# Kernel optimization log

Measured on AMD Instinct MI355X. Metric: run time of the kernel, lower is better.

## Reference

```python
import jax, jax.numpy as jnp
import numpy as np

N_NODES = 262144
N_EDGES = 4194304
F_IN = 4
HID = 8
HEADS = 2
N_CLS = 3
NEG_SLOPE = 0.2
EPS = 1e-16


def setup_inputs() -> dict:
    key = jax.random.key(0)
    k = jax.random.split(key, 8)
    x = jax.random.normal(k[0], (N_NODES, F_IN), dtype=jnp.float32)
    edge_index = jax.random.randint(k[1], (2, N_EDGES), 0, N_NODES, dtype=jnp.int64)
    # layer 1: in=4, heads=2, out=8, concat -> 16
    W1 = jax.random.normal(k[2], (F_IN, HEADS * HID), dtype=jnp.float32) * 0.5
    a_src1 = jax.random.normal(k[3], (HEADS, HID), dtype=jnp.float32) * 0.5
    a_dst1 = jax.random.normal(k[4], (HEADS, HID), dtype=jnp.float32) * 0.5
    # layer 2: in=16, heads=1, out=3, mean (concat=False)
    W2 = jax.random.normal(k[5], (HEADS * HID, 1 * N_CLS), dtype=jnp.float32) * 0.5
    a_src2 = jax.random.normal(k[6], (1, N_CLS), dtype=jnp.float32) * 0.5
    a_dst2 = jax.random.normal(k[7], (1, N_CLS), dtype=jnp.float32) * 0.5
    return {"x": x, "edge_index": edge_index, "W1": W1, "a_src1": a_src1,
            "a_dst1": a_dst1, "W2": W2, "a_src2": a_src2, "a_dst2": a_dst2}


def _gat_conv(x, src, dst, W, a_src, a_dst, heads, out_dim, concat):
    N = x.shape[0]
    h = (x @ W).reshape(N, heads, out_dim)            # [N,H,F]
    al_s = jnp.sum(h * a_src[None], axis=-1)          # [N,H]
    al_d = jnp.sum(h * a_dst[None], axis=-1)          # [N,H]
    e = jax.nn.leaky_relu(al_s[src] + al_d[dst], NEG_SLOPE)  # [E,H]
    m = jax.ops.segment_max(e, dst, num_segments=N)   # [N,H]
    ex = jnp.exp(e - m[dst])
    denom = jax.ops.segment_sum(ex, dst, num_segments=N)
    alpha = ex / (denom[dst] + EPS)                   # [E,H]
    out = jax.ops.segment_sum(h[src] * alpha[:, :, None], dst, num_segments=N)  # [N,H,F]
    if concat:
        return out.reshape(N, heads * out_dim)
    return out.mean(axis=1)


def reference(x, edge_index, W1, a_src1, a_dst1, W2, a_src2, a_dst2):
    N = x.shape[0]
    loops = jnp.arange(N, dtype=edge_index.dtype)
    src = jnp.concatenate([edge_index[0], loops])
    dst = jnp.concatenate([edge_index[1], loops])
    h = _gat_conv(x, src, dst, W1, a_src1, a_dst1, HEADS, HID, True)
    h = jax.nn.relu(h)
    out = _gat_conv(h, src, dst, W2, a_src2, a_dst2, 1, N_CLS, False)
    return jax.nn.softmax(out, axis=-1)
```

## Files before the change

### kernel.cpp

```cpp
#include <hip/hip_runtime.h>
#include <cstdint>
#include <cstddef>


#define NN 262144
#define NE 4194304
#define NB 1024
#define NPB 256
#define EB 8192
#define NBLK (NE / EB)
#define CAPB 4608
#define BT 512
#define ILEN (CAPB / BT)

__device__ __forceinline__ float lrelu(float v) { return v > 0.0f ? v : 0.2f * v; }
__device__ __forceinline__ float rfl(float v) {
    return __int_as_float(__builtin_amdgcn_readfirstlane(__float_as_int(v)));
}

__global__ __launch_bounds__(512, 8) void k_bin(const void* __restrict__ ei,
                                                unsigned* __restrict__ binned,
                                                unsigned* __restrict__ runs)
{
    __shared__ unsigned stage[EB];
    __shared__ int h[NB];
    __shared__ int wtot[8];
    __shared__ int sfmt;
    int t = threadIdx.x, blk = blockIdx.x;
    for (int i = t; i < NB; i += 512) h[i] = 0;
    if (t == 0) {
        const unsigned* u = (const unsigned*)ei;
        int is64 = 1;
        for (int k = 0; k < 64; ++k)
            if (u[2 * k + 1] != 0u) { is64 = 0; break; }
        sfmt = is64;
    }
    __syncthreads();
    int f64 = sfmt;
    size_t base = (size_t)blk * EB;
    int dd[16], ss[16];
    if (f64) {
        const long long* ps = (const long long*)ei;
        const long long* pd = ps + NE;
#pragma unroll
        for (int r = 0; r < 16; ++r) {
            size_t e = base + (size_t)r * 512 + t;
            ss[r] = (int)ps[e];
            dd[r] = (int)pd[e];
            atomicAdd(&h[dd[r] >> 8], 1);
        }
    } else {
        const int* ps = (const int*)ei;
        const int* pd = ps + NE;
#pragma unroll
        for (int r = 0; r < 16; ++r) {
            size_t e = base + (size_t)r * 512 + t;
            ss[r] = ps[e];
            dd[r] = pd[e];
            atomicAdd(&h[dd[r] >> 8], 1);
        }
    }
    __syncthreads();
    int c0 = h[2 * t], c1 = h[2 * t + 1];
    int own = c0 + c1;
    int lane = t & 63, w = t >> 6;
    int p = own;
#pragma unroll
    for (int o = 1; o < 64; o <<= 1) {
        int v = __shfl_up(p, o);
        if (lane >= o) p += v;
    }
    if (lane == 63) wtot[w] = p;
    __syncthreads();
    int bw = 0;
#pragma unroll
    for (int q = 0; q < 8; ++q) bw += (q < w) ? wtot[q] : 0;
    int e0 = bw + p - own;
    h[2 * t] = e0;
    h[2 * t + 1] = e0 + c0;
    ((uint2*)(runs + (size_t)blk * NB))[t] =
        make_uint2((unsigned)e0 | ((unsigned)c0 << 16),
                   (unsigned)(e0 + c0) | ((unsigned)c1 << 16));
    __syncthreads();
#pragma unroll
    for (int r = 0; r < 16; ++r) {
        int pos = atomicAdd(&h[dd[r] >> 8], 1);
        stage[pos] = ((unsigned)(dd[r] & 255) << 18) | (unsigned)ss[r];
    }
    __syncthreads();
    uint4* dst4 = (uint4*)(binned + (size_t)blk * EB);
    const uint4* src4 = (const uint4*)stage;
    for (int i = t; i < EB / 4; i += 512) dst4[i] = src4[i];
}

__global__ __launch_bounds__(256) void k_truns(const unsigned* __restrict__ runs,
                                               unsigned* __restrict__ runsT)
{
    __shared__ unsigned tile[32][33];
    int tx = threadIdx.x & 31, ty = threadIdx.x >> 5;
    int bx = blockIdx.x * 32;
    int by = blockIdx.y * 32;
#pragma unroll
    for (int j = 0; j < 4; ++j)
        tile[ty + 8 * j][tx] = runs[(size_t)(by + ty + 8 * j) * NB + bx + tx];
    __syncthreads();
#pragma unroll
    for (int j = 0; j < 4; ++j)
        runsT[(size_t)(bx + ty + 8 * j) * NBLK + by + tx] = tile[tx][ty + 8 * j];
}

__global__ __launch_bounds__(BT, 8) void k_l1f(
    const float4* __restrict__ x4,
    const float* __restrict__ W1, const float* __restrict__ as1, const float* __restrict__ ad1,
    const unsigned* __restrict__ binned, const unsigned* __restrict__ runsT,
    const float* __restrict__ W2, const float* __restrict__ as2, const float* __restrict__ ad2,
    int* __restrict__ ssrc, int2* __restrict__ rse,
    float4* __restrict__ p4, float* __restrict__ ald2)
{
    __shared__ unsigned stage[CAPB];
    __shared__ int pf[NBLK + 1];
    __shared__ int gb[NBLK];
    __shared__ int hist[NPB], off[NPB], rsL[NPB], reL[NPB];
    __shared__ int wt1[8], wt2[4];
    __shared__ float sW1[64], sW2[48], sf[16], sa2[6];
    int t = threadIdx.x, b = blockIdx.x;
    if (t < 64) sW1[t] = W1[t];
    if (t >= 64 && t < 112) sW2[t - 64] = W2[t - 64];
    if (t >= 128 && t < 144) {
        int i = t - 128;
        int kind = i >> 3, head = (i >> 2) & 1, f = i & 3;
        const float* a = kind ? ad1 : as1;
        float v = 0.f;
        for (int j = 0; j < 8; ++j)
            v += W1[f * 16 + head * 8 + j] * a[head * 8 + j];
        sf[i] = v;
    }
    if (t >= 144 && t < 147) sa2[t - 144] = as2[t - 144];
    if (t >= 147 && t < 150) sa2[t - 144] = ad2[t - 147];
    if (t < NPB) hist[t] = 0;
    unsigned rn = runsT[(size_t)b * NBLK + t];
    int cnt = (int)(rn >> 16);
    int lane = t & 63, w = t >> 6;
    int p = cnt;
#pragma unroll
    for (int o = 1; o < 64; o <<= 1) {
        int v = __shfl_up(p, o);
        if (lane >= o) p += v;
    }
    if (lane == 63) wt1[w] = p;
    __syncthreads();
    int bw = 0;
#pragma unroll
    for (int q = 0; q < 8; ++q) bw += (q < w) ? wt1[q] : 0;
    int incl = bw + p;
    int excl = incl - cnt;
    pf[t] = excl;
    if (t == BT - 1) pf[NBLK] = incl;
    gb[t] = t * EB + (int)(rn & 0xFFFF);
    __syncthreads();
    int n = pf[NBLK] < CAPB ? pf[NBLK] : CAPB;
    unsigned pk[ILEN];
#pragma unroll
    for (int k = 0; k < ILEN; ++k) {
        int i = k * BT + t;
        pk[k] = 0xFFFFFFFFu;
        if (i < n) {
            int r = 0;
#pragma unroll
            for (int s = 256; s > 0; s >>= 1)
                if (pf[r + s] <= i) r += s;
            unsigned pp = binned[gb[r] + (i - pf[r])];
            pk[k] = pp;
            atomicAdd(&hist[pp >> 18], 1);
        }
    }
    __syncthreads();
    int ownN = (t < NPB) ? hist[t] : 0;
    int pN = ownN;
#pragma unroll
    for (int o = 1; o < 64; o <<= 1) {
        int v = __shfl_up(pN, o);
        if (lane >= o) pN += v;
    }
    if (t < NPB && lane == 63) wt2[w] = pN;
    __syncthreads();
    int s0 = b * CAPB;
    if (t < NPB) {
        int baseN = 0;
#pragma unroll
        for (int q = 0; q < 4; ++q) baseN += (q < w) ? wt2[q] : 0;
        int exclN = baseN + pN - ownN;
        off[t] = exclN;
        rsL[t] = exclN;
        reL[t] = exclN + ownN;
        rse[b * NPB + t] = make_int2(s0 + exclN, s0 + exclN + ownN);
    }
    __syncthreads();
#pragma unroll
    for (int k = 0; k < ILEN; ++k) {
        unsigned pp = pk[k];
        if (pp != 0xFFFFFFFFu) {
            int pos = atomicAdd(&off[pp >> 18], 1);
            stage[pos] = pp & 0x3FFFFu;
        }
    }
    __syncthreads();
    for (int i = t; i < n; i += BT) ssrc[s0 + i] = (int)stage[i];
    float ws00 = rfl(sf[0]),  ws01 = rfl(sf[1]),  ws02 = rfl(sf[2]),  ws03 = rfl(sf[3]);
    float ws10 = rfl(sf[4]),  ws11 = rfl(sf[5]),  ws12 = rfl(sf[6]),  ws13 = rfl(sf[7]);
    float wd00 = rfl(sf[8]),  wd01 = rfl(sf[9]),  wd02 = rfl(sf[10]), wd03 = rfl(sf[11]);
    float wd10 = rfl(sf[12]), wd11 = rfl(sf[13]), wd12 = rfl(sf[14]), wd13 = rfl(sf[15]);
    int nl = t >> 1, sub = t & 1;
    int node = b * NPB + nl;
    float4 xn = x4[node];
    float ald0  = xn.x * wd00 + xn.y * wd01 + xn.z * wd02 + xn.w * wd03;
    float ald1v = xn.x * wd10 + xn.y * wd11 + xn.z * wd12 + xn.w * wd13;
    float den0 = 0.f, den1 = 0.f;
    float wa00 = 0.f, wa01 = 0.f, wa02 = 0.f, wa03 = 0.f;
    float wa10 = 0.f, wa11 = 0.f, wa12 = 0.f, wa13 = 0.f;
    if (sub == 0) {
        float as0s = xn.x * ws00 + xn.y * ws01 + xn.z * ws02 + xn.w * ws03;
        float as1s = xn.x * ws10 + xn.y * ws11 + xn.z * ws12 + xn.w * ws13;
        float x0 = __expf(lrelu(as0s + ald0));
        float x1 = __expf(lrelu(as1s + ald1v));
        den0 = x0; den1 = x1;
        wa00 = x0 * xn.x; wa01 = x0 * xn.y; wa02 = x0 * xn.z; wa03 = x0 * xn.w;
        wa10 = x1 * xn.x; wa11 = x1 * xn.y; wa12 = x1 * xn.z; wa13 = x1 * xn.w;
    }
    int j = rsL[nl] + sub, je = reL[nl];
    float4 xsA, xsB;
    if (j < je) xsA = x4[stage[j]];
    if (j + 2 < je) xsB = x4[stage[j + 2]];
    while (j < je) {
        float4 xs = xsA;
        xsA = xsB;
        if (j + 4 < je) xsB = x4[stage[j + 4]];
        float as0 = xs.x * ws00 + xs.y * ws01 + xs.z * ws02 + xs.w * ws03;
        float as1v = xs.x * ws10 + xs.y * ws11 + xs.z * ws12 + xs.w * ws13;
        float e0 = __expf(lrelu(as0 + ald0));
        float e1 = __expf(lrelu(as1v + ald1v));
        den0 += e0; den1 += e1;
        wa00 += e0 * xs.x; wa01 += e0 * xs.y; wa02 += e0 * xs.z; wa03 += e0 * xs.w;
        wa10 += e1 * xs.x; wa11 += e1 * xs.y; wa12 += e1 * xs.z; wa13 += e1 * xs.w;
        j += 2;
    }
    den0 += __shfl_xor(den0, 1);  den1 += __shfl_xor(den1, 1);
    wa00 += __shfl_xor(wa00, 1);  wa01 += __shfl_xor(wa01, 1);
    wa02 += __shfl_xor(wa02, 1);  wa03 += __shfl_xor(wa03, 1);
    wa10 += __shfl_xor(wa10, 1);  wa11 += __shfl_xor(wa11, 1);
    wa12 += __shfl_xor(wa12, 1);  wa13 += __shfl_xor(wa13, 1);
    if (sub == 0) {
        float i0 = 1.0f / (den0 + 1e-16f);
        float i1 = 1.0f / (den1 + 1e-16f);
        float p0 = 0.f, p1 = 0.f, p2 = 0.f;
#pragma unroll
        for (int f = 0; f < 8; ++f) {
            float num0 = wa00 * sW1[f]      + wa01 * sW1[16 + f]
                       + wa02 * sW1[32 + f] + wa03 * sW1[48 + f];
            float num1 = wa10 * sW1[8 + f]  + wa11 * sW1[24 + f]
                       + wa12 * sW1[40 + f] + wa13 * sW1[56 + f];
            float o0 = fmaxf(num0 * i0, 0.f);
            float o1 = fmaxf(num1 * i1, 0.f);
            p0 += o0 * sW2[f * 3 + 0] + o1 * sW2[(8 + f) * 3 + 0];
            p1 += o0 * sW2[f * 3 + 1] + o1 * sW2[(8 + f) * 3 + 1];
            p2 += o0 * sW2[f * 3 + 2] + o1 * sW2[(8 + f) * 3 + 2];
        }
        float als2v = p0 * sa2[0] + p1 * sa2[1] + p2 * sa2[2];
        float ald2v = p0 * sa2[3] + p1 * sa2[4] + p2 * sa2[5];
        p4[node] = make_float4(als2v, p0, p1, p2);
        ald2[node] = ald2v;
    }
}

__global__ __launch_bounds__(BT, 8) void k_l2agg(
    const float4* __restrict__ p4, const float* __restrict__ ald2,
    const int2* __restrict__ rse, const int* __restrict__ ssrc,
    float* __restrict__ out)
{
    __shared__ unsigned stage[CAPB];
    __shared__ int rsL[NPB], reL[NPB];
    __shared__ int sn;
    int t = threadIdx.x, b = blockIdx.x;
    int s0 = b * CAPB;
    if (t < NPB) {
        int2 se = rse[b * NPB + t];
        rsL[t] = se.x - s0;
        reL[t] = se.y - s0;
        if (t == NPB - 1) sn = se.y - s0;
    }
    __syncthreads();
    int n = sn;
    for (int i = t; i < n; i += BT) stage[i] = (unsigned)ssrc[s0 + i];
    __syncthreads();
    int nl = t >> 1, sub = t & 1;
    int node = b * NPB + nl;
    float aldi = ald2[node];
    float den = 0.f, a0 = 0.f, a1 = 0.f, a2 = 0.f;
    if (sub == 0) {
        float4 pn = p4[node];
        float xv = __expf(lrelu(pn.x + aldi));
        den = xv; a0 = xv * pn.y; a1 = xv * pn.z; a2 = xv * pn.w;
    }
    int j = rsL[nl] + sub, je = reL[nl];
    float4 pA, pB;
    if (j < je) pA = p4[stage[j]];
    if (j + 2 < je) pB = p4[stage[j + 2]];
    while (j < je) {
        float4 pv = pA;
        pA = pB;
        if (j + 4 < je) pB = p4[stage[j + 4]];
        float e = __expf(lrelu(pv.x + aldi));
        den += e; a0 += e * pv.y; a1 += e * pv.z; a2 += e * pv.w;
        j += 2;
    }
    den += __shfl_xor(den, 1);
    a0 += __shfl_xor(a0, 1);
    a1 += __shfl_xor(a1, 1);
    a2 += __shfl_xor(a2, 1);
    if (sub == 0) {
        float inv = 1.0f / (den + 1e-16f);
        float l0 = a0 * inv, l1 = a1 * inv, l2 = a2 * inv;
        float m = fmaxf(l0, fmaxf(l1, l2));
        float e0 = __expf(l0 - m), e1 = __expf(l1 - m), e2 = __expf(l2 - m);
        float is = 1.0f / (e0 + e1 + e2);
        out[(size_t)node * 3 + 0] = e0 * is;
        out[(size_t)node * 3 + 1] = e1 * is;
        out[(size_t)node * 3 + 2] = e2 * is;
    }
}

extern "C" void kernel_launch(void* const* d_in, const int* in_sizes, int n_in,
                              void* d_out, int out_size, void* d_ws, size_t ws_size,
                              hipStream_t stream)
{
    const float* x   = (const float*)d_in[0];
    const void*  ei  = d_in[1];
    const float* W1  = (const float*)d_in[2];
    const float* as1 = (const float*)d_in[3];
    const float* ad1 = (const float*)d_in[4];
    const float* W2  = (const float*)d_in[5];
    const float* as2 = (const float*)d_in[6];
    const float* ad2 = (const float*)d_in[7];
    float* out = (float*)d_out;

    char* ws = (char*)d_ws;
    size_t off = 0;
    auto carve = [&](size_t bytes) {
        void* p = ws + off;
        off = (off + bytes + 255) & ~(size_t)255;
        return p;
    };
    unsigned* binned = (unsigned*)carve((size_t)NE * 4);
    unsigned* runs   = (unsigned*)carve((size_t)NBLK * NB * 4);
    unsigned* runsT  = (unsigned*)carve((size_t)NB * NBLK * 4);
    int*      ssrc   = (int*)carve((size_t)NB * CAPB * 4);
    int2*     rse    = (int2*)carve((size_t)NN * 8);
    float4*   p4     = (float4*)carve((size_t)NN * 16);
    float*    ald2   = (float*)carve((size_t)NN * 4);

    k_bin<<<NBLK, 512, 0, stream>>>(ei, binned, runs);
    k_truns<<<dim3(NB / 32, NBLK / 32), 256, 0, stream>>>(runs, runsT);
    k_l1f<<<NB, BT, 0, stream>>>((const float4*)x, W1, as1, ad1, binned, runsT,
                                 W2, as2, ad2, ssrc, rse, p4, ald2);
    k_l2agg<<<NB, BT, 0, stream>>>(p4, ald2, rse, ssrc, out);
}
```

Baseline: 86.78 us.

## Sort nodes by in-degree within each block to balance per-wave edge loops

Each block now buckets its 256 nodes by in-degree (capped at 63) with a shared-memory histogram and prefix scan. Threads process nodes in that sorted order in both the layer-1 fused kernel and the layer-2 aggregation kernel, so lanes within a wavefront have similar loop trip counts and less divergence. The local node id is packed into the top 8 bits of the range start, and layer 2 finds the segment end with an atomicMax. This adds extra syncs, atomics and an indirection, and it assumes segment offsets fit in 24 bits.

```diff
diff --git a/kernel.cpp b/kernel.cpp
--- a/kernel.cpp
+++ b/kernel.cpp
@@ -122,9 +122,11 @@
     __shared__ int gb[NBLK];
     __shared__ int hist[NPB], off[NPB], rsL[NPB], reL[NPB];
     __shared__ int wt1[8], wt2[4];
+    __shared__ int dbin[64], dcur[64];
+    __shared__ unsigned ord[NPB];
     __shared__ float sW1[64], sW2[48], sf[16], sa2[6];
     int t = threadIdx.x, b = blockIdx.x;
-    if (t < 64) sW1[t] = W1[t];
+    if (t < 64) { sW1[t] = W1[t]; dbin[t] = 0; }
     if (t >= 64 && t < 112) sW2[t - 64] = W2[t - 64];
     if (t >= 128 && t < 144) {
         int i = t - 128;
@@ -185,6 +187,7 @@
     if (t < NPB && lane == 63) wt2[w] = pN;
     __syncthreads();
     int s0 = b * CAPB;
+    int myDeg = 0;
     if (t < NPB) {
         int baseN = 0;
 #pragma unroll
@@ -193,9 +196,20 @@
         off[t] = exclN;
         rsL[t] = exclN;
         reL[t] = exclN + ownN;
-        rse[b * NPB + t] = make_int2(s0 + exclN, s0 + exclN + ownN);
-    }
-    __syncthreads();
+        myDeg = ownN < 63 ? ownN : 63;
+        atomicAdd(&dbin[myDeg], 1);
+    }
+    __syncthreads();
+    if (t < 64) {
+        int v = dbin[t];
+        int pb = v;
+#pragma unroll
+        for (int o = 1; o < 64; o <<= 1) {
+            int u = __shfl_up(pb, o);
+            if (t >= o) pb += u;
+        }
+        dcur[t] = pb - v;
+    }
 #pragma unroll
     for (int k = 0; k < ILEN; ++k) {
         unsigned pp = pk[k];
@@ -205,13 +219,22 @@
         }
     }
     __syncthreads();
+    if (t < NPB) {
+        int rank = atomicAdd(&dcur[myDeg], 1);
+        ord[rank] = (unsigned)t;
+        rse[b * NPB + rank] =
+            make_int2((int)(((unsigned)(s0 + rsL[t])) | ((unsigned)t << 24)),
+                      s0 + reL[t]);
+    }
     for (int i = t; i < n; i += BT) ssrc[s0 + i] = (int)stage[i];
+    __syncthreads();
     float ws00 = rfl(sf[0]),  ws01 = rfl(sf[1]),  ws02 = rfl(sf[2]),  ws03 = rfl(sf[3]);
     float ws10 = rfl(sf[4]),  ws11 = rfl(sf[5]),  ws12 = rfl(sf[6]),  ws13 = rfl(sf[7]);
     float wd00 = rfl(sf[8]),  wd01 = rfl(sf[9]),  wd02 = rfl(sf[10]), wd03 = rfl(sf[11]);
     float wd10 = rfl(sf[12]), wd11 = rfl(sf[13]), wd12 = rfl(sf[14]), wd13 = rfl(sf[15]);
     int nl = t >> 1, sub = t & 1;
-    int node = b * NPB + nl;
+    int nloc = (int)ord[nl];
+    int node = b * NPB + nloc;
     float4 xn = x4[node];
     float ald0  = xn.x * wd00 + xn.y * wd01 + xn.z * wd02 + xn.w * wd03;
     float ald1v = xn.x * wd10 + xn.y * wd11 + xn.z * wd12 + xn.w * wd13;
@@ -227,7 +250,7 @@
         wa00 = x0 * xn.x; wa01 = x0 * xn.y; wa02 = x0 * xn.z; wa03 = x0 * xn.w;
         wa10 = x1 * xn.x; wa11 = x1 * xn.y; wa12 = x1 * xn.z; wa13 = x1 * xn.w;
     }
-    int j = rsL[nl] + sub, je = reL[nl];
+    int j = rsL[nloc] + sub, je = reL[nloc];
     float4 xsA, xsB;
     if (j < je) xsA = x4[stage[j]];
     if (j + 2 < je) xsB = x4[stage[j + 2]];
@@ -278,22 +301,26 @@
     float* __restrict__ out)
 {
     __shared__ unsigned stage[CAPB];
-    __shared__ int rsL[NPB], reL[NPB];
+    __shared__ int rsL[NPB], reL[NPB], ndL[NPB];
     __shared__ int sn;
     int t = threadIdx.x, b = blockIdx.x;
     int s0 = b * CAPB;
+    if (t == 0) sn = 0;
+    __syncthreads();
     if (t < NPB) {
         int2 se = rse[b * NPB + t];
-        rsL[t] = se.x - s0;
+        unsigned ux = (unsigned)se.x;
+        rsL[t] = (int)(ux & 0xFFFFFFu) - s0;
         reL[t] = se.y - s0;
-        if (t == NPB - 1) sn = se.y - s0;
+        ndL[t] = (int)(ux >> 24);
+        atomicMax(&sn, se.y - s0);
     }
     __syncthreads();
     int n = sn;
     for (int i = t; i < n; i += BT) stage[i] = (unsigned)ssrc[s0 + i];
     __syncthreads();
     int nl = t >> 1, sub = t & 1;
-    int node = b * NPB + nl;
+    int node = b * NPB + ndL[nl];
     float aldi = ald2[node];
     float den = 0.f, a0 = 0.f, a1 = 0.f, a2 = 0.f;
     if (sub == 0) {
```

New measurement: 93.43 us. 1.08x slower.

## Stage gathered source features into LDS in chunks before per-node aggregation

Applied to the files above, without the earlier changes.

Both aggregation kernels now gather the source-node float4 features cooperatively into a shared-memory buffer, in four chunks of 1152 edges, and then each thread pair reads its edges from LDS. Before, each thread pair walked its own edge list with register double-buffering. The goal is to flatten load imbalance across nodes with uneven degree and to issue coalesced, evenly spread gather loads. The cost is extra block-wide barriers, 18KB more LDS per block, which may reduce occupancy, and a loss of overlap between loads and compute.

```diff
diff --git a/kernel.cpp b/kernel.cpp
--- a/kernel.cpp
+++ b/kernel.cpp
@@ -12,6 +12,7 @@
 #define CAPB 4608
 #define BT 512
 #define ILEN (CAPB / BT)
+#define QE 1152
 
 __device__ __forceinline__ float lrelu(float v) { return v > 0.0f ? v : 0.2f * v; }
 __device__ __forceinline__ float rfl(float v) {
@@ -118,6 +119,7 @@
     float4* __restrict__ p4, float* __restrict__ ald2)
 {
     __shared__ unsigned stage[CAPB];
+    __shared__ float4 xbuf[QE];
     __shared__ int pf[NBLK + 1];
     __shared__ int gb[NBLK];
     __shared__ int hist[NPB], off[NPB], rsL[NPB], reL[NPB];
@@ -227,22 +229,28 @@
         wa00 = x0 * xn.x; wa01 = x0 * xn.y; wa02 = x0 * xn.z; wa03 = x0 * xn.w;
         wa10 = x1 * xn.x; wa11 = x1 * xn.y; wa12 = x1 * xn.z; wa13 = x1 * xn.w;
     }
-    int j = rsL[nl] + sub, je = reL[nl];
-    float4 xsA, xsB;
-    if (j < je) xsA = x4[stage[j]];
-    if (j + 2 < je) xsB = x4[stage[j + 2]];
-    while (j < je) {
-        float4 xs = xsA;
-        xsA = xsB;
-        if (j + 4 < je) xsB = x4[stage[j + 4]];
-        float as0 = xs.x * ws00 + xs.y * ws01 + xs.z * ws02 + xs.w * ws03;
-        float as1v = xs.x * ws10 + xs.y * ws11 + xs.z * ws12 + xs.w * ws13;
-        float e0 = __expf(lrelu(as0 + ald0));
-        float e1 = __expf(lrelu(as1v + ald1v));
-        den0 += e0; den1 += e1;
-        wa00 += e0 * xs.x; wa01 += e0 * xs.y; wa02 += e0 * xs.z; wa03 += e0 * xs.w;
-        wa10 += e1 * xs.x; wa11 += e1 * xs.y; wa12 += e1 * xs.z; wa13 += e1 * xs.w;
-        j += 2;
+    int rs = rsL[nl], re = reL[nl];
+    for (int q = 0; q < 4; ++q) {
+        int q0 = q * QE, q1 = q0 + QE;
+        __syncthreads();
+        for (int i = t; i < QE; i += BT) {
+            int g = q0 + i;
+            if (g < n) xbuf[i] = x4[stage[g]];
+        }
+        __syncthreads();
+        int jb = rs > q0 ? rs : q0;
+        jb += ((jb - rs) & 1) ^ sub;
+        int je = re < q1 ? re : q1;
+        for (int j = jb; j < je; j += 2) {
+            float4 xs = xbuf[j - q0];
+            float as0 = xs.x * ws00 + xs.y * ws01 + xs.z * ws02 + xs.w * ws03;
+            float as1v = xs.x * ws10 + xs.y * ws11 + xs.z * ws12 + xs.w * ws13;
+            float e0 = __expf(lrelu(as0 + ald0));
+            float e1 = __expf(lrelu(as1v + ald1v));
+            den0 += e0; den1 += e1;
+            wa00 += e0 * xs.x; wa01 += e0 * xs.y; wa02 += e0 * xs.z; wa03 += e0 * xs.w;
+            wa10 += e1 * xs.x; wa11 += e1 * xs.y; wa12 += e1 * xs.z; wa13 += e1 * xs.w;
+        }
     }
     den0 += __shfl_xor(den0, 1);  den1 += __shfl_xor(den1, 1);
     wa00 += __shfl_xor(wa00, 1);  wa01 += __shfl_xor(wa01, 1);
@@ -278,6 +286,7 @@
     float* __restrict__ out)
 {
     __shared__ unsigned stage[CAPB];
+    __shared__ float4 pbuf[QE];
     __shared__ int rsL[NPB], reL[NPB];
     __shared__ int sn;
     int t = threadIdx.x, b = blockIdx.x;
@@ -291,7 +300,6 @@
     __syncthreads();
     int n = sn;
     for (int i = t; i < n; i += BT) stage[i] = (unsigned)ssrc[s0 + i];
-    __syncthreads();
     int nl = t >> 1, sub = t & 1;
     int node = b * NPB + nl;
     float aldi = ald2[node];
@@ -301,17 +309,24 @@
         float xv = __expf(lrelu(pn.x + aldi));
         den = xv; a0 = xv * pn.y; a1 = xv * pn.z; a2 = xv * pn.w;
     }
-    int j = rsL[nl] + sub, je = reL[nl];
-    float4 pA, pB;
-    if (j < je) pA = p4[stage[j]];
-    if (j + 2 < je) pB = p4[stage[j + 2]];
-    while (j < je) {
-        float4 pv = pA;
-        pA = pB;
-        if (j + 4 < je) pB = p4[stage[j + 4]];
-        float e = __expf(lrelu(pv.x + aldi));
-        den += e; a0 += e * pv.y; a1 += e * pv.z; a2 += e * pv.w;
-        j += 2;
+    __syncthreads();
+    int rs = rsL[nl], re = reL[nl];
+    for (int q = 0; q < 4; ++q) {
+        int q0 = q * QE, q1 = q0 + QE;
+        if (q) __syncthreads();
+        for (int i = t; i < QE; i += BT) {
+            int g = q0 + i;
+            if (g < n) pbuf[i] = p4[stage[g]];
+        }
+        __syncthreads();
+        int jb = rs > q0 ? rs : q0;
+        jb += ((jb - rs) & 1) ^ sub;
+        int je = re < q1 ? re : q1;
+        for (int j = jb; j < je; j += 2) {
+            float4 pv = pbuf[j - q0];
+            float e = __expf(lrelu(pv.x + aldi));
+            den += e; a0 += e * pv.y; a1 += e * pv.z; a2 += e * pv.w;
+        }
     }
     den += __shfl_xor(den, 1);
     a0 += __shfl_xor(a0, 1);
```

Result: slower. 106.8 us (+23.0%).

## Split fused sort+layer-1 kernel and deepen gather prefetch to four stages

Applied to the files above, without the earlier changes.

Splits the combined bucket-sort and layer-1 aggregation kernel into a separate sort kernel that writes sorted sources and ranges, and an aggregation kernel that reloads them from global memory into shared memory. It also deepens the software prefetch of neighbour feature gathers from two to four in-flight loads in both aggregation loops. The goal is to lower per-kernel register and shared-memory pressure and hide more gather latency. The cost is an extra launch plus an extra global round trip of the sorted index array, and more registers held by the deeper prefetch.

```diff
diff --git a/kernel.cpp b/kernel.cpp
--- a/kernel.cpp
+++ b/kernel.cpp
@@ -109,21 +109,98 @@
         runsT[(size_t)(bx + ty + 8 * j) * NBLK + by + tx] = tile[tx][ty + 8 * j];
 }
 
-__global__ __launch_bounds__(BT, 8) void k_l1f(
-    const float4* __restrict__ x4,
-    const float* __restrict__ W1, const float* __restrict__ as1, const float* __restrict__ ad1,
+__global__ __launch_bounds__(BT, 8) void k_sort(
     const unsigned* __restrict__ binned, const unsigned* __restrict__ runsT,
-    const float* __restrict__ W2, const float* __restrict__ as2, const float* __restrict__ ad2,
-    int* __restrict__ ssrc, int2* __restrict__ rse,
-    float4* __restrict__ p4, float* __restrict__ ald2)
+    int* __restrict__ ssrc, int2* __restrict__ rse)
 {
     __shared__ unsigned stage[CAPB];
     __shared__ int pf[NBLK + 1];
     __shared__ int gb[NBLK];
-    __shared__ int hist[NPB], off[NPB], rsL[NPB], reL[NPB];
+    __shared__ int hist[NPB], off[NPB];
     __shared__ int wt1[8], wt2[4];
+    int t = threadIdx.x, b = blockIdx.x;
+    if (t < NPB) hist[t] = 0;
+    unsigned rn = runsT[(size_t)b * NBLK + t];
+    int cnt = (int)(rn >> 16);
+    int lane = t & 63, w = t >> 6;
+    int p = cnt;
+#pragma unroll
+    for (int o = 1; o < 64; o <<= 1) {
+        int v = __shfl_up(p, o);
+        if (lane >= o) p += v;
+    }
+    if (lane == 63) wt1[w] = p;
+    __syncthreads();
+    int bw = 0;
+#pragma unroll
+    for (int q = 0; q < 8; ++q) bw += (q < w) ? wt1[q] : 0;
+    int incl = bw + p;
+    int excl = incl - cnt;
+    pf[t] = excl;
+    if (t == BT - 1) pf[NBLK] = incl;
+    gb[t] = t * EB + (int)(rn & 0xFFFF);
+    __syncthreads();
+    int n = pf[NBLK] < CAPB ? pf[NBLK] : CAPB;
+    unsigned pk[ILEN];
+#pragma unroll
+    for (int k = 0; k < ILEN; ++k) {
+        int i = k * BT + t;
+        pk[k] = 0xFFFFFFFFu;
+        if (i < n) {
+            int r = 0;
+#pragma unroll
+            for (int s = 256; s > 0; s >>= 1)
+                if (pf[r + s] <= i) r += s;
+            unsigned pp = binned[gb[r] + (i - pf[r])];
+            pk[k] = pp;
+            atomicAdd(&hist[pp >> 18], 1);
+        }
+    }
+    __syncthreads();
+    int ownN = (t < NPB) ? hist[t] : 0;
+    int pN = ownN;
+#pragma unroll
+    for (int o = 1; o < 64; o <<= 1) {
+        int v = __shfl_up(pN, o);
+        if (lane >= o) pN += v;
+    }
+    if (t < NPB && lane == 63) wt2[w] = pN;
+    __syncthreads();
+    int s0 = b * CAPB;
+    if (t < NPB) {
+        int baseN = 0;
+#pragma unroll
+        for (int q = 0; q < 4; ++q) baseN += (q < w) ? wt2[q] : 0;
+        int exclN = baseN + pN - ownN;
+        off[t] = exclN;
+        rse[b * NPB + t] = make_int2(s0 + exclN, s0 + exclN + ownN);
+    }
+    __syncthreads();
+#pragma unroll
+    for (int k = 0; k < ILEN; ++k) {
+        unsigned pp = pk[k];
+        if (pp != 0xFFFFFFFFu) {
+            int pos = atomicAdd(&off[pp >> 18], 1);
+            stage[pos] = pp & 0x3FFFFu;
+        }
+    }
+    __syncthreads();
+    for (int i = t; i < n; i += BT) ssrc[s0 + i] = (int)stage[i];
+}
+
+__global__ __launch_bounds__(BT, 8) void k_agg(
+    const float4* __restrict__ x4,
+    const float* __restrict__ W1, const float* __restrict__ as1, const float* __restrict__ ad1,
+    const float* __restrict__ W2, const float* __restrict__ as2, const float* __restrict__ ad2,
+    const int* __restrict__ ssrc, const int2* __restrict__ rse,
+    float4* __restrict__ p4, float* __restrict__ ald2)
+{
+    __shared__ unsigned stage[CAPB];
+    __shared__ int rsL[NPB], reL[NPB];
     __shared__ float sW1[64], sW2[48], sf[16], sa2[6];
+    __shared__ int sn;
     int t = threadIdx.x, b = blockIdx.x;
+    int s0 = b * CAPB;
     if (t < 64) sW1[t] = W1[t];
     if (t >= 64 && t < 112) sW2[t - 64] = W2[t - 64];
     if (t >= 128 && t < 144) {
@@ -137,75 +214,16 @@
     }
     if (t >= 144 && t < 147) sa2[t - 144] = as2[t - 144];
     if (t >= 147 && t < 150) sa2[t - 144] = ad2[t - 147];
-    if (t < NPB) hist[t] = 0;
-    unsigned rn = runsT[(size_t)b * NBLK + t];
-    int cnt = (int)(rn >> 16);
-    int lane = t & 63, w = t >> 6;
-    int p = cnt;
-#pragma unroll
-    for (int o = 1; o < 64; o <<= 1) {
-        int v = __shfl_up(p, o);
-        if (lane >= o) p += v;
-    }
-    if (lane == 63) wt1[w] = p;
-    __syncthreads();
-    int bw = 0;
-#pragma unroll
-    for (int q = 0; q < 8; ++q) bw += (q < w) ? wt1[q] : 0;
-    int incl = bw + p;
-    int excl = incl - cnt;
-    pf[t] = excl;
-    if (t == BT - 1) pf[NBLK] = incl;
-    gb[t] = t * EB + (int)(rn & 0xFFFF);
-    __syncthreads();
-    int n = pf[NBLK] < CAPB ? pf[NBLK] : CAPB;
-    unsigned pk[ILEN];
-#pragma unroll
-    for (int k = 0; k < ILEN; ++k) {
-        int i = k * BT + t;
-        pk[k] = 0xFFFFFFFFu;
-        if (i < n) {
-            int r = 0;
-#pragma unroll
-            for (int s = 256; s > 0; s >>= 1)
-                if (pf[r + s] <= i) r += s;
-            unsigned pp = binned[gb[r] + (i - pf[r])];
-            pk[k] = pp;
-            atomicAdd(&hist[pp >> 18], 1);
-        }
-    }
-    __syncthreads();
-    int ownN = (t < NPB) ? hist[t] : 0;
-    int pN = ownN;
-#pragma unroll
-    for (int o = 1; o < 64; o <<= 1) {
-        int v = __shfl_up(pN, o);
-        if (lane >= o) pN += v;
-    }
-    if (t < NPB && lane == 63) wt2[w] = pN;
-    __syncthreads();
-    int s0 = b * CAPB;
     if (t < NPB) {
-        int baseN = 0;
-#pragma unroll
-        for (int q = 0; q < 4; ++q) baseN += (q < w) ? wt2[q] : 0;
-        int exclN = baseN + pN - ownN;
-        off[t] = exclN;
-        rsL[t] = exclN;
-        reL[t] = exclN + ownN;
-        rse[b * NPB + t] = make_int2(s0 + exclN, s0 + exclN + ownN);
-    }
-    __syncthreads();
-#pragma unroll
-    for (int k = 0; k < ILEN; ++k) {
-        unsigned pp = pk[k];
-        if (pp != 0xFFFFFFFFu) {
-            int pos = atomicAdd(&off[pp >> 18], 1);
-            stage[pos] = pp & 0x3FFFFu;
-        }
-    }
-    __syncthreads();
-    for (int i = t; i < n; i += BT) ssrc[s0 + i] = (int)stage[i];
+        int2 se = rse[b * NPB + t];
+        rsL[t] = se.x - s0;
+        reL[t] = se.y - s0;
+        if (t == NPB - 1) sn = se.y - s0;
+    }
+    __syncthreads();
+    int n = sn;
+    for (int i = t; i < n; i += BT) stage[i] = (unsigned)ssrc[s0 + i];
+    __syncthreads();
     float ws00 = rfl(sf[0]),  ws01 = rfl(sf[1]),  ws02 = rfl(sf[2]),  ws03 = rfl(sf[3]);
     float ws10 = rfl(sf[4]),  ws11 = rfl(sf[5]),  ws12 = rfl(sf[6]),  ws13 = rfl(sf[7]);
     float wd00 = rfl(sf[8]),  wd01 = rfl(sf[9]),  wd02 = rfl(sf[10]), wd03 = rfl(sf[11]);
@@ -228,13 +246,15 @@
         wa10 = x1 * xn.x; wa11 = x1 * xn.y; wa12 = x1 * xn.z; wa13 = x1 * xn.w;
     }
     int j = rsL[nl] + sub, je = reL[nl];
-    float4 xsA, xsB;
+    float4 xsA, xsB, xsC, xsD;
     if (j < je) xsA = x4[stage[j]];
     if (j + 2 < je) xsB = x4[stage[j + 2]];
+    if (j + 4 < je) xsC = x4[stage[j + 4]];
+    if (j + 6 < je) xsD = x4[stage[j + 6]];
     while (j < je) {
         float4 xs = xsA;
-        xsA = xsB;
-        if (j + 4 < je) xsB = x4[stage[j + 4]];
+        xsA = xsB; xsB = xsC; xsC = xsD;
+        if (j + 8 < je) xsD = x4[stage[j + 8]];
         float as0 = xs.x * ws00 + xs.y * ws01 + xs.z * ws02 + xs.w * ws03;
         float as1v = xs.x * ws10 + xs.y * ws11 + xs.z * ws12 + xs.w * ws13;
         float e0 = __expf(lrelu(as0 + ald0));
@@ -302,13 +322,15 @@
         den = xv; a0 = xv * pn.y; a1 = xv * pn.z; a2 = xv * pn.w;
     }
     int j = rsL[nl] + sub, je = reL[nl];
-    float4 pA, pB;
+    float4 pA, pB, pC, pD;
     if (j < je) pA = p4[stage[j]];
     if (j + 2 < je) pB = p4[stage[j + 2]];
+    if (j + 4 < je) pC = p4[stage[j + 4]];
+    if (j + 6 < je) pD = p4[stage[j + 6]];
     while (j < je) {
         float4 pv = pA;
-        pA = pB;
-        if (j + 4 < je) pB = p4[stage[j + 4]];
+        pA = pB; pB = pC; pC = pD;
+        if (j + 8 < je) pD = p4[stage[j + 8]];
         float e = __expf(lrelu(pv.x + aldi));
         den += e; a0 += e * pv.y; a1 += e * pv.z; a2 += e * pv.w;
         j += 2;
@@ -360,7 +382,8 @@
 
     k_bin<<<NBLK, 512, 0, stream>>>(ei, binned, runs);
     k_truns<<<dim3(NB / 32, NBLK / 32), 256, 0, stream>>>(runs, runsT);
-    k_l1f<<<NB, BT, 0, stream>>>((const float4*)x, W1, as1, ad1, binned, runsT,
+    k_sort<<<NB, BT, 0, stream>>>(binned, runsT, ssrc, rse);
+    k_agg<<<NB, BT, 0, stream>>>((const float4*)x, W1, as1, ad1,
                                  W2, as2, ad2, ssrc, rse, p4, ald2);
     k_l2agg<<<NB, BT, 0, stream>>>(p4, ald2, rse, ssrc, out);
 }
```

Measured after the change: 94.58 us. +9.0%, slower.
